# Kernel optimization log

Measured on AMD Instinct MI355X. Metric: run time of the kernel, lower is better.

## Reference

```python
import jax, jax.numpy as jnp
import numpy as np

U, I, D, E, B = 100000, 50000, 128, 3200000, 4096
KEEP_PROB = 0.8

def setup_inputs() -> dict:
    key = jax.random.key(0)
    ks = jax.random.split(key, 9)
    return {
        "user_emb": 0.01 * jax.random.normal(ks[0], (U, D), dtype=jnp.float32),
        "item_emb": 0.01 * jax.random.normal(ks[1], (I, D), dtype=jnp.float32),
        "vals": jax.random.uniform(ks[2], (E,), dtype=jnp.float32),
        "keep_mask": jax.random.uniform(ks[3], (E,), dtype=jnp.float32),
        "rows": jax.random.randint(ks[4], (E,), 0, U, dtype=jnp.int32),
        "cols": jax.random.randint(ks[5], (E,), 0, I, dtype=jnp.int32),
        "user": jax.random.randint(ks[6], (B,), 0, U, dtype=jnp.int32),
        "pos_item": jax.random.randint(ks[7], (B,), 0, I, dtype=jnp.int32),
        "neg_item": jax.random.randint(ks[8], (B,), 0, I, dtype=jnp.int32),
    }

def reference(user_emb, item_emb, vals, keep_mask, rows, cols, user, pos_item, neg_item):
    # Edge dropout: keep edge iff uniform < keep_prob, rescale by 1/keep_prob.
    # (Equivalent to torch's index filtering, expressed as zeroed values.)
    dvals = jnp.where(keep_mask < KEEP_PROB, vals / KEEP_PROB, 0.0)
    u0, i0 = user_emb, item_emb
    # i_1 = spmm(A^T, u_0): scatter edge messages by item (col) index.  [I, D]
    i1 = jax.ops.segment_sum(dvals[:, None] * u0[rows], cols, num_segments=item_emb.shape[0])
    # u_1 = spmm(A, i_0): scatter edge messages by user (row) index.    [U, D]
    u1 = jax.ops.segment_sum(dvals[:, None] * i0[cols], rows, num_segments=user_emb.shape[0])
    # Layer combination (mean of layer-0 and layer-1), gathered per batch.
    u = (u0[user] + u1[user]) * 0.5        # [B, D]
    i = (i0[pos_item] + i1[pos_item]) * 0.5
    j = (i0[neg_item] + i1[neg_item]) * 0.5
    pos_score = jnp.sum(u * i, axis=1, keepdims=True)  # [B, 1]
    neg_score = jnp.sum(u * j, axis=1, keepdims=True)  # [B, 1]
    return (pos_score, neg_score)
```

## Files before the change

kernel.cpp:

```cpp
#include <hip/hip_runtime.h>

#define DIM 128
#define KEEP_PROB 0.8f
#define UCAP 96
#define ICAP 160

__global__ void init_ws_kernel(int4* slots, int slot_vecs, int4* ctrs, int ctr_vecs) {
    int stride = gridDim.x * blockDim.x;
    int t = blockIdx.x * blockDim.x + threadIdx.x;
    int4 m1 = make_int4(-1, -1, -1, -1);
    for (int i = t; i < slot_vecs; i += stride) slots[i] = m1;
    int4 z = make_int4(0, 0, 0, 0);
    for (int i = t; i < ctr_vecs; i += stride) ctrs[i] = z;
}

__global__ void slot_kernel(const int* __restrict__ user, const int* __restrict__ pos,
                            const int* __restrict__ neg, int* __restrict__ u_slot,
                            int* __restrict__ i_slot, int B) {
    int t = blockIdx.x * blockDim.x + threadIdx.x;
    if (t < B) {
        u_slot[user[t]] = t;
    } else if (t < 2 * B) {
        i_slot[pos[t - B]] = t - B;
    } else if (t < 3 * B) {
        i_slot[neg[t - 2 * B]] = (t - 2 * B) + B;
    }
}

__global__ void fill_bucket_kernel(const float* __restrict__ vals, const float* __restrict__ keep,
                                   const int* __restrict__ rows, const int* __restrict__ cols,
                                   const int* __restrict__ u_slot, const int* __restrict__ i_slot,
                                   int* __restrict__ cursor, int2* __restrict__ entries,
                                   int E, int B) {
    int t = blockIdx.x * blockDim.x + threadIdx.x;
    int base = t * 4;
    if (base >= E) return;
    long long ibase = (long long)B * UCAP;
    if (base + 3 < E) {
        float4 km = *(const float4*)(keep + base);
        float4 vv = *(const float4*)(vals + base);
        int4 r4 = *(const int4*)(rows + base);
        int4 c4 = *(const int4*)(cols + base);
        float k[4] = {km.x, km.y, km.z, km.w};
        float v[4] = {vv.x, vv.y, vv.z, vv.w};
        int rr[4] = {r4.x, r4.y, r4.z, r4.w};
        int cc[4] = {c4.x, c4.y, c4.z, c4.w};
#pragma unroll
        for (int j = 0; j < 4; j++) {
            if (k[j] < KEEP_PROB) {
                float dv = v[j] * 1.25f;
                int us = u_slot[rr[j]];
                if (us >= 0) {
                    int p = atomicAdd(&cursor[us], 1);
                    if (p < UCAP) entries[(long long)us * UCAP + p] = make_int2(cc[j], __float_as_int(dv));
                }
                int is = i_slot[cc[j]];
                if (is >= 0) {
                    int p = atomicAdd(&cursor[B + is], 1);
                    if (p < ICAP) entries[ibase + (long long)is * ICAP + p] = make_int2(rr[j], __float_as_int(dv));
                }
            }
        }
    } else {
        for (int e = base; e < E; e++) {
            if (keep[e] < KEEP_PROB) {
                float dv = vals[e] * 1.25f;
                int us = u_slot[rows[e]];
                if (us >= 0) {
                    int p = atomicAdd(&cursor[us], 1);
                    if (p < UCAP) entries[(long long)us * UCAP + p] = make_int2(cols[e], __float_as_int(dv));
                }
                int is = i_slot[cols[e]];
                if (is >= 0) {
                    int p = atomicAdd(&cursor[B + is], 1);
                    if (p < ICAP) entries[ibase + (long long)is * ICAP + p] = make_int2(rows[e], __float_as_int(dv));
                }
            }
        }
    }
}

__global__ void count_kernel(const float* __restrict__ keep, const int* __restrict__ rows,
                             const int* __restrict__ cols, const int* __restrict__ u_slot,
                             const int* __restrict__ i_slot, int* __restrict__ cnt,
                             int E, int B) {
    int t = blockIdx.x * blockDim.x + threadIdx.x;
    int base = t * 4;
    if (base >= E) return;
    if (base + 3 < E) {
        float4 km = *(const float4*)(keep + base);
        int4 r4 = *(const int4*)(rows + base);
        int4 c4 = *(const int4*)(cols + base);
        float k[4] = {km.x, km.y, km.z, km.w};
        int rr[4] = {r4.x, r4.y, r4.z, r4.w};
        int cc[4] = {c4.x, c4.y, c4.z, c4.w};
#pragma unroll
        for (int j = 0; j < 4; j++) {
            if (k[j] < KEEP_PROB) {
                int us = u_slot[rr[j]];
                if (us >= 0) atomicAdd(&cnt[us], 1);
                int is = i_slot[cc[j]];
                if (is >= 0) atomicAdd(&cnt[B + is], 1);
            }
        }
    } else {
        for (int e = base; e < E; e++) {
            if (keep[e] < KEEP_PROB) {
                int us = u_slot[rows[e]];
                if (us >= 0) atomicAdd(&cnt[us], 1);
                int is = i_slot[cols[e]];
                if (is >= 0) atomicAdd(&cnt[B + is], 1);
            }
        }
    }
}

__global__ void scan_kernel(const int* __restrict__ cnt, int* __restrict__ offs,
                            int* __restrict__ cursor, int n) {
    __shared__ int wave_tot[16];
    __shared__ int carry_s;
    int tid = threadIdx.x, lane = tid & 63, wv = tid >> 6;
    if (tid == 0) carry_s = 0;
    __syncthreads();
    for (int base = 0; base < n; base += 1024) {
        int v = (base + tid < n) ? cnt[base + tid] : 0;
        int x = v;
#pragma unroll
        for (int off = 1; off < 64; off <<= 1) {
            int y = __shfl_up(x, off);
            if (lane >= off) x += y;
        }
        if (lane == 63) wave_tot[wv] = x;
        __syncthreads();
        if (wv == 0 && lane < 16) {
            int tot = wave_tot[lane];
            int s = tot;
#pragma unroll
            for (int off = 1; off < 16; off <<= 1) {
                int y = __shfl_up(s, off);
                if (lane >= off) s += y;
            }
            wave_tot[lane] = s - tot;
        }
        __syncthreads();
        int excl = (x - v) + wave_tot[wv] + carry_s;
        if (base + tid < n) { offs[base + tid] = excl; cursor[base + tid] = excl; }
        __syncthreads();
        if (tid == 1023) carry_s += wave_tot[15] + x;
        __syncthreads();
    }
}

__global__ void fill_csr_kernel(const float* __restrict__ vals, const float* __restrict__ keep,
                                const int* __restrict__ rows, const int* __restrict__ cols,
                                const int* __restrict__ u_slot, const int* __restrict__ i_slot,
                                int* __restrict__ cursor, int2* __restrict__ entries,
                                long long cap, int E, int B) {
    int t = blockIdx.x * blockDim.x + threadIdx.x;
    int base = t * 4;
    if (base >= E) return;
    if (base + 3 < E) {
        float4 km = *(const float4*)(keep + base);
        float4 vv = *(const float4*)(vals + base);
        int4 r4 = *(const int4*)(rows + base);
        int4 c4 = *(const int4*)(cols + base);
        float k[4] = {km.x, km.y, km.z, km.w};
        float v[4] = {vv.x, vv.y, vv.z, vv.w};
        int rr[4] = {r4.x, r4.y, r4.z, r4.w};
        int cc[4] = {c4.x, c4.y, c4.z, c4.w};
#pragma unroll
        for (int j = 0; j < 4; j++) {
            if (k[j] < KEEP_PROB) {
                float dv = v[j] * 1.25f;
                int us = u_slot[rr[j]];
                if (us >= 0) {
                    int p = atomicAdd(&cursor[us], 1);
                    if (p < cap) entries[p] = make_int2(cc[j], __float_as_int(dv));
                }
                int is = i_slot[cc[j]];
                if (is >= 0) {
                    int p = atomicAdd(&cursor[B + is], 1);
                    if (p < cap) entries[p] = make_int2(rr[j], __float_as_int(dv));
                }
            }
        }
    } else {
        for (int e = base; e < E; e++) {
            if (keep[e] < KEEP_PROB) {
                float dv = vals[e] * 1.25f;
                int us = u_slot[rows[e]];
                if (us >= 0) {
                    int p = atomicAdd(&cursor[us], 1);
                    if (p < cap) entries[p] = make_int2(cols[e], __float_as_int(dv));
                }
                int is = i_slot[cols[e]];
                if (is >= 0) {
                    int p = atomicAdd(&cursor[B + is], 1);
                    if (p < cap) entries[p] = make_int2(rows[e], __float_as_int(dv));
                }
            }
        }
    }
}

__global__ void gather_kernel(const int2* __restrict__ entries, const int* __restrict__ offs,
                              const int* __restrict__ cntp, const float* __restrict__ u0,
                              const float* __restrict__ i0, float* __restrict__ u1c,
                              float* __restrict__ i1c, int B, int mode, long long cap) {
    int wave = (blockIdx.x * blockDim.x + threadIdx.x) >> 6;
    int lane = threadIdx.x & 63;
    if (wave >= 3 * B) return;
    const float* table;
    float* dst;
    if (wave < B) { table = i0; dst = u1c + (size_t)wave * DIM; }
    else          { table = u0; dst = i1c + (size_t)(wave - B) * DIM; }

    int n = cntp[wave];
    long long base;
    if (mode == 1) {
        if (wave < B) { base = (long long)wave * UCAP; if (n > UCAP) n = UCAP; }
        else          { base = (long long)B * UCAP + (long long)(wave - B) * ICAP; if (n > ICAP) n = ICAP; }
    } else {
        base = offs[wave];
        if (base + n > cap) n = (int)(cap - base < 0 ? 0 : cap - base);
    }

    int o = lane * 2;
    float ax = 0.f, ay = 0.f;
    for (int k0 = 0; k0 < n; k0 += 64) {
        int idx = k0 + lane;
        int2 e = make_int2(0, 0);
        if (idx < n) e = entries[base + idx];
        int m = n - k0;
        if (m > 64) m = 64;
        int j = 0;
        for (; j + 4 <= m; j += 4) {
            int s0 = __shfl(e.x, j + 0), s1 = __shfl(e.x, j + 1);
            int s2 = __shfl(e.x, j + 2), s3 = __shfl(e.x, j + 3);
            float d0 = __int_as_float(__shfl(e.y, j + 0));
            float d1 = __int_as_float(__shfl(e.y, j + 1));
            float d2 = __int_as_float(__shfl(e.y, j + 2));
            float d3 = __int_as_float(__shfl(e.y, j + 3));
            float2 r0 = *(const float2*)(table + (size_t)s0 * DIM + o);
            float2 r1 = *(const float2*)(table + (size_t)s1 * DIM + o);
            float2 r2 = *(const float2*)(table + (size_t)s2 * DIM + o);
            float2 r3 = *(const float2*)(table + (size_t)s3 * DIM + o);
            ax += d0 * r0.x; ay += d0 * r0.y;
            ax += d1 * r1.x; ay += d1 * r1.y;
            ax += d2 * r2.x; ay += d2 * r2.y;
            ax += d3 * r3.x; ay += d3 * r3.y;
        }
        for (; j < m; j++) {
            int s = __shfl(e.x, j);
            float dv = __int_as_float(__shfl(e.y, j));
            float2 r = *(const float2*)(table + (size_t)s * DIM + o);
            ax += dv * r.x; ay += dv * r.y;
        }
    }
    *(float2*)(dst + o) = make_float2(ax, ay);
}

__global__ void score_kernel(const float* __restrict__ u0, const float* __restrict__ i0,
                             const float* __restrict__ u1c, const float* __restrict__ i1c,
                             const int* __restrict__ user, const int* __restrict__ pos,
                             const int* __restrict__ neg, const int* __restrict__ u_slot,
                             const int* __restrict__ i_slot, float* __restrict__ out, int B) {
    int wave = (blockIdx.x * blockDim.x + threadIdx.x) >> 6;
    int lane = threadIdx.x & 63;
    if (wave >= B) return;

    int ub = user[wave], pb = pos[wave], nb = neg[wave];
    int usl = u_slot[ub], psl = i_slot[pb], nsl = i_slot[nb];
    int o = lane * 2;

    float2 a0 = *(const float2*)(u0  + (size_t)ub  * DIM + o);
    float2 a1 = *(const float2*)(u1c + (size_t)usl * DIM + o);
    float2 p0 = *(const float2*)(i0  + (size_t)pb  * DIM + o);
    float2 p1 = *(const float2*)(i1c + (size_t)psl * DIM + o);
    float2 n0 = *(const float2*)(i0  + (size_t)nb  * DIM + o);
    float2 n1 = *(const float2*)(i1c + (size_t)nsl * DIM + o);

    float ux = (a0.x + a1.x) * 0.5f, uy = (a0.y + a1.y) * 0.5f;
    float px = (p0.x + p1.x) * 0.5f, py = (p0.y + p1.y) * 0.5f;
    float nx = (n0.x + n1.x) * 0.5f, ny = (n0.y + n1.y) * 0.5f;

    float ps = ux * px + uy * py;
    float ns = ux * nx + uy * ny;
    for (int off = 32; off > 0; off >>= 1) {
        ps += __shfl_down(ps, off);
        ns += __shfl_down(ns, off);
    }
    if (lane == 0) {
        out[wave]     = ps;
        out[B + wave] = ns;
    }
}

extern "C" void kernel_launch(void* const* d_in, const int* in_sizes, int n_in,
                              void* d_out, int out_size, void* d_ws, size_t ws_size,
                              hipStream_t stream) {
    const float* user_emb = (const float*)d_in[0];
    const float* item_emb = (const float*)d_in[1];
    const float* vals     = (const float*)d_in[2];
    const float* keep     = (const float*)d_in[3];
    const int*   rows     = (const int*)d_in[4];
    const int*   cols     = (const int*)d_in[5];
    const int*   user     = (const int*)d_in[6];
    const int*   pos      = (const int*)d_in[7];
    const int*   neg      = (const int*)d_in[8];
    float* out = (float*)d_out;

    int U = in_sizes[0] / DIM;
    int I = in_sizes[1] / DIM;
    int E = in_sizes[2];
    int B = in_sizes[6];

    char* p = (char*)d_ws;
    int* u_slot = (int*)p;              p += (size_t)U * 4;
    int* i_slot = (int*)p;              p += (size_t)I * 4;
    int* cnt    = (int*)p;              p += (size_t)3 * B * 4;
    int* offs   = (int*)p;              p += (size_t)3 * B * 4;
    int* cursor = (int*)p;              p += (size_t)3 * B * 4;
    float* u1c  = (float*)p;            p += (size_t)B * DIM * 4;
    float* i1c  = (float*)p;            p += (size_t)2 * B * DIM * 4;
    int2* entries = (int2*)p;
    size_t used = (size_t)(p - (char*)d_ws);
    long long avail = (long long)ws_size - (long long)used;

    long long bucket_entries = (long long)B * UCAP + (long long)2 * B * ICAP;
    int mode = (avail >= bucket_entries * (long long)sizeof(int2)) ? 1 : 0;

    int slot_vecs = (U + I) / 4;
    int ctr_vecs  = (9 * B) / 4;

    init_ws_kernel<<<256, 256, 0, stream>>>((int4*)u_slot, slot_vecs, (int4*)cnt, ctr_vecs);
    slot_kernel<<<(3 * B + 255) / 256, 256, 0, stream>>>(user, pos, neg, u_slot, i_slot, B);

    int scan_threads = (E + 3) / 4;
    int scan_blocks = (scan_threads + 255) / 256;

    long long cap;
    if (mode == 1) {
        cap = bucket_entries;
        fill_bucket_kernel<<<scan_blocks, 256, 0, stream>>>(vals, keep, rows, cols, u_slot,
                                                            i_slot, cursor, entries, E, B);
        gather_kernel<<<(3 * B * 64 + 255) / 256, 256, 0, stream>>>(entries, offs, cursor,
                                                                    user_emb, item_emb, u1c,
                                                                    i1c, B, 1, cap);
    } else {
        cap = avail / (long long)sizeof(int2);
        if (cap < 0) cap = 0;
        count_kernel<<<scan_blocks, 256, 0, stream>>>(keep, rows, cols, u_slot, i_slot, cnt, E, B);
        scan_kernel<<<1, 1024, 0, stream>>>(cnt, offs, cursor, 3 * B);
        fill_csr_kernel<<<scan_blocks, 256, 0, stream>>>(vals, keep, rows, cols, u_slot, i_slot,
                                                         cursor, entries, cap, E, B);
        gather_kernel<<<(3 * B * 64 + 255) / 256, 256, 0, stream>>>(entries, offs, cnt,
                                                                    user_emb, item_emb, u1c,
                                                                    i1c, B, 0, cap);
    }

    score_kernel<<<(B * 64 + 255) / 256, 256, 0, stream>>>(user_emb, item_emb, u1c, i1c,
                                                           user, pos, neg, u_slot, i_slot,
                                                           out, B);
}
```

Before: 227.9 us.

## Filter edges with membership bitmasks and split gather rows across two waves

Adds compact bitmasks of the batch users and items, built in the slot kernel. The fill kernel now tests a small, cache-resident bitmask before touching the large slot arrays, and each of its threads handles 8 edges instead of 4. The gather kernel assigns two waves per destination row, interleaving the row's entries between them, unrolling by 8 and combining the two halves through shared memory. The init kernel is replaced by memsets. The fallback CSR kernels are simplified to scalar loops, and the gather grid assumes 3*B is even.

```diff
diff --git a/kernel.cpp b/kernel.cpp
--- a/kernel.cpp
+++ b/kernel.cpp
@@ -5,75 +5,77 @@
 #define UCAP 96
 #define ICAP 160
 
-__global__ void init_ws_kernel(int4* slots, int slot_vecs, int4* ctrs, int ctr_vecs) {
-    int stride = gridDim.x * blockDim.x;
-    int t = blockIdx.x * blockDim.x + threadIdx.x;
-    int4 m1 = make_int4(-1, -1, -1, -1);
-    for (int i = t; i < slot_vecs; i += stride) slots[i] = m1;
-    int4 z = make_int4(0, 0, 0, 0);
-    for (int i = t; i < ctr_vecs; i += stride) ctrs[i] = z;
-}
-
 __global__ void slot_kernel(const int* __restrict__ user, const int* __restrict__ pos,
                             const int* __restrict__ neg, int* __restrict__ u_slot,
-                            int* __restrict__ i_slot, int B) {
+                            int* __restrict__ i_slot, unsigned* __restrict__ u_mask,
+                            unsigned* __restrict__ i_mask, int B) {
     int t = blockIdx.x * blockDim.x + threadIdx.x;
     if (t < B) {
-        u_slot[user[t]] = t;
+        int u = user[t];
+        u_slot[u] = t;
+        atomicOr(&u_mask[u >> 5], 1u << (u & 31));
     } else if (t < 2 * B) {
-        i_slot[pos[t - B]] = t - B;
+        int it = pos[t - B];
+        i_slot[it] = t - B;
+        atomicOr(&i_mask[it >> 5], 1u << (it & 31));
     } else if (t < 3 * B) {
-        i_slot[neg[t - 2 * B]] = (t - 2 * B) + B;
+        int it = neg[t - 2 * B];
+        i_slot[it] = (t - 2 * B) + B;
+        atomicOr(&i_mask[it >> 5], 1u << (it & 31));
     }
 }
 
 __global__ void fill_bucket_kernel(const float* __restrict__ vals, const float* __restrict__ keep,
                                    const int* __restrict__ rows, const int* __restrict__ cols,
                                    const int* __restrict__ u_slot, const int* __restrict__ i_slot,
+                                   const unsigned* __restrict__ u_mask,
+                                   const unsigned* __restrict__ i_mask,
                                    int* __restrict__ cursor, int2* __restrict__ entries,
                                    int E, int B) {
     int t = blockIdx.x * blockDim.x + threadIdx.x;
-    int base = t * 4;
+    int base = t * 8;
     if (base >= E) return;
-    long long ibase = (long long)B * UCAP;
-    if (base + 3 < E) {
-        float4 km = *(const float4*)(keep + base);
-        float4 vv = *(const float4*)(vals + base);
-        int4 r4 = *(const int4*)(rows + base);
-        int4 c4 = *(const int4*)(cols + base);
-        float k[4] = {km.x, km.y, km.z, km.w};
-        float v[4] = {vv.x, vv.y, vv.z, vv.w};
-        int rr[4] = {r4.x, r4.y, r4.z, r4.w};
-        int cc[4] = {c4.x, c4.y, c4.z, c4.w};
+    long long ib = (long long)B * UCAP;
+    if (base + 7 < E) {
+        float4 ka = *(const float4*)(keep + base), kb = *(const float4*)(keep + base + 4);
+        float4 va = *(const float4*)(vals + base), vb = *(const float4*)(vals + base + 4);
+        int4 ra = *(const int4*)(rows + base), rb = *(const int4*)(rows + base + 4);
+        int4 ca = *(const int4*)(cols + base), cb = *(const int4*)(cols + base + 4);
+        float kk[8] = {ka.x, ka.y, ka.z, ka.w, kb.x, kb.y, kb.z, kb.w};
+        float vv[8] = {va.x, va.y, va.z, va.w, vb.x, vb.y, vb.z, vb.w};
+        int rr[8] = {ra.x, ra.y, ra.z, ra.w, rb.x, rb.y, rb.z, rb.w};
+        int cc[8] = {ca.x, ca.y, ca.z, ca.w, cb.x, cb.y, cb.z, cb.w};
 #pragma unroll
-        for (int j = 0; j < 4; j++) {
-            if (k[j] < KEEP_PROB) {
-                float dv = v[j] * 1.25f;
-                int us = u_slot[rr[j]];
-                if (us >= 0) {
+        for (int j = 0; j < 8; j++) {
+            if (kk[j] < KEEP_PROB) {
+                int r = rr[j], c = cc[j];
+                float dv = vv[j] * 1.25f;
+                if ((u_mask[r >> 5] >> (r & 31)) & 1u) {
+                    int us = u_slot[r];
                     int p = atomicAdd(&cursor[us], 1);
-                    if (p < UCAP) entries[(long long)us * UCAP + p] = make_int2(cc[j], __float_as_int(dv));
+                    if (p < UCAP) entries[(long long)us * UCAP + p] = make_int2(c, __float_as_int(dv));
                 }
-                int is = i_slot[cc[j]];
-                if (is >= 0) {
+                if ((i_mask[c >> 5] >> (c & 31)) & 1u) {
+                    int is = i_slot[c];
                     int p = atomicAdd(&cursor[B + is], 1);
-                    if (p < ICAP) entries[ibase + (long long)is * ICAP + p] = make_int2(rr[j], __float_as_int(dv));
+                    if (p < ICAP) entries[ib + (long long)is * ICAP + p] = make_int2(r, __float_as_int(dv));
                 }
             }
         }
     } else {
         for (int e = base; e < E; e++) {
             if (keep[e] < KEEP_PROB) {
+                int r = rows[e], c = cols[e];
                 float dv = vals[e] * 1.25f;
-                int us = u_slot[rows[e]];
-                if (us >= 0) {
+                if ((u_mask[r >> 5] >> (r & 31)) & 1u) {
+                    int us = u_slot[r];
                     int p = atomicAdd(&cursor[us], 1);
-                    if (p < UCAP) entries[(long long)us * UCAP + p] = make_int2(cols[e], __float_as_int(dv));
+                    if (p < UCAP) entries[(long long)us * UCAP + p] = make_int2(c, __float_as_int(dv));
                 }
-                int is = i_slot[cols[e]];
-                if (is >= 0) {
+                if ((i_mask[c >> 5] >> (c & 31)) & 1u) {
+                    int is = i_slot[c];
                     int p = atomicAdd(&cursor[B + is], 1);
-                    if (p < ICAP) entries[ibase + (long long)is * ICAP + p] = make_int2(rows[e], __float_as_int(dv));
+                    if (p < ICAP) entries[ib + (long long)is * ICAP + p] = make_int2(r, __float_as_int(dv));
                 }
             }
         }
@@ -87,30 +89,12 @@
     int t = blockIdx.x * blockDim.x + threadIdx.x;
     int base = t * 4;
     if (base >= E) return;
-    if (base + 3 < E) {
-        float4 km = *(const float4*)(keep + base);
-        int4 r4 = *(const int4*)(rows + base);
-        int4 c4 = *(const int4*)(cols + base);
-        float k[4] = {km.x, km.y, km.z, km.w};
-        int rr[4] = {r4.x, r4.y, r4.z, r4.w};
-        int cc[4] = {c4.x, c4.y, c4.z, c4.w};
-#pragma unroll
-        for (int j = 0; j < 4; j++) {
-            if (k[j] < KEEP_PROB) {
-                int us = u_slot[rr[j]];
-                if (us >= 0) atomicAdd(&cnt[us], 1);
-                int is = i_slot[cc[j]];
-                if (is >= 0) atomicAdd(&cnt[B + is], 1);
-            }
-        }
-    } else {
-        for (int e = base; e < E; e++) {
-            if (keep[e] < KEEP_PROB) {
-                int us = u_slot[rows[e]];
-                if (us >= 0) atomicAdd(&cnt[us], 1);
-                int is = i_slot[cols[e]];
-                if (is >= 0) atomicAdd(&cnt[B + is], 1);
-            }
+    for (int e = base; e < base + 4 && e < E; e++) {
+        if (keep[e] < KEEP_PROB) {
+            int us = u_slot[rows[e]];
+            if (us >= 0) atomicAdd(&cnt[us], 1);
+            int is = i_slot[cols[e]];
+            if (is >= 0) atomicAdd(&cnt[B + is], 1);
         }
     }
 }
@@ -159,45 +143,18 @@
     int t = blockIdx.x * blockDim.x + threadIdx.x;
     int base = t * 4;
     if (base >= E) return;
-    if (base + 3 < E) {
-        float4 km = *(const float4*)(keep + base);
-        float4 vv = *(const float4*)(vals + base);
-        int4 r4 = *(const int4*)(rows + base);
-        int4 c4 = *(const int4*)(cols + base);
-        float k[4] = {km.x, km.y, km.z, km.w};
-        float v[4] = {vv.x, vv.y, vv.z, vv.w};
-        int rr[4] = {r4.x, r4.y, r4.z, r4.w};
-        int cc[4] = {c4.x, c4.y, c4.z, c4.w};
-#pragma unroll
-        for (int j = 0; j < 4; j++) {
-            if (k[j] < KEEP_PROB) {
-                float dv = v[j] * 1.25f;
-                int us = u_slot[rr[j]];
-                if (us >= 0) {
-                    int p = atomicAdd(&cursor[us], 1);
-                    if (p < cap) entries[p] = make_int2(cc[j], __float_as_int(dv));
-                }
-                int is = i_slot[cc[j]];
-                if (is >= 0) {
-                    int p = atomicAdd(&cursor[B + is], 1);
-                    if (p < cap) entries[p] = make_int2(rr[j], __float_as_int(dv));
-                }
-            }
-        }
-    } else {
-        for (int e = base; e < E; e++) {
-            if (keep[e] < KEEP_PROB) {
-                float dv = vals[e] * 1.25f;
-                int us = u_slot[rows[e]];
-                if (us >= 0) {
-                    int p = atomicAdd(&cursor[us], 1);
-                    if (p < cap) entries[p] = make_int2(cols[e], __float_as_int(dv));
-                }
-                int is = i_slot[cols[e]];
-                if (is >= 0) {
-                    int p = atomicAdd(&cursor[B + is], 1);
-                    if (p < cap) entries[p] = make_int2(rows[e], __float_as_int(dv));
-                }
+    for (int e = base; e < base + 4 && e < E; e++) {
+        if (keep[e] < KEEP_PROB) {
+            float dv = vals[e] * 1.25f;
+            int us = u_slot[rows[e]];
+            if (us >= 0) {
+                int p = atomicAdd(&cursor[us], 1);
+                if (p < cap) entries[p] = make_int2(cols[e], __float_as_int(dv));
+            }
+            int is = i_slot[cols[e]];
+            if (is >= 0) {
+                int p = atomicAdd(&cursor[B + is], 1);
+                if (p < cap) entries[p] = make_int2(rows[e], __float_as_int(dv));
             }
         }
     }
@@ -207,57 +164,81 @@
                               const int* __restrict__ cntp, const float* __restrict__ u0,
                               const float* __restrict__ i0, float* __restrict__ u1c,
                               float* __restrict__ i1c, int B, int mode, long long cap) {
-    int wave = (blockIdx.x * blockDim.x + threadIdx.x) >> 6;
+    __shared__ float part[2][DIM];
+    int pair = threadIdx.x >> 7;
+    int half = (threadIdx.x >> 6) & 1;
     int lane = threadIdx.x & 63;
-    if (wave >= 3 * B) return;
+    int dest = blockIdx.x * 2 + pair;
+
     const float* table;
     float* dst;
-    if (wave < B) { table = i0; dst = u1c + (size_t)wave * DIM; }
-    else          { table = u0; dst = i1c + (size_t)(wave - B) * DIM; }
-
-    int n = cntp[wave];
+    if (dest < B) { table = i0; dst = u1c + (size_t)dest * DIM; }
+    else          { table = u0; dst = i1c + (size_t)(dest - B) * DIM; }
+
+    int n = cntp[dest];
     long long base;
     if (mode == 1) {
-        if (wave < B) { base = (long long)wave * UCAP; if (n > UCAP) n = UCAP; }
-        else          { base = (long long)B * UCAP + (long long)(wave - B) * ICAP; if (n > ICAP) n = ICAP; }
+        if (dest < B) { base = (long long)dest * UCAP; if (n > UCAP) n = UCAP; }
+        else { base = (long long)B * UCAP + (long long)(dest - B) * ICAP; if (n > ICAP) n = ICAP; }
     } else {
-        base = offs[wave];
-        if (base + n > cap) n = (int)(cap - base < 0 ? 0 : cap - base);
-    }
-
+        base = offs[dest];
+        if (base + n > cap) { long long rem = cap - base; n = rem < 0 ? 0 : (int)rem; }
+    }
+
+    int m = (n - half + 1) >> 1;
     int o = lane * 2;
     float ax = 0.f, ay = 0.f;
-    for (int k0 = 0; k0 < n; k0 += 64) {
-        int idx = k0 + lane;
+    for (int k0 = 0; k0 < m; k0 += 64) {
+        int my = k0 + lane;
         int2 e = make_int2(0, 0);
-        if (idx < n) e = entries[base + idx];
-        int m = n - k0;
-        if (m > 64) m = 64;
+        if (my < m) e = entries[base + half + 2 * (long long)my];
+        int mm = m - k0;
+        if (mm > 64) mm = 64;
         int j = 0;
-        for (; j + 4 <= m; j += 4) {
+        for (; j + 8 <= mm; j += 8) {
             int s0 = __shfl(e.x, j + 0), s1 = __shfl(e.x, j + 1);
             int s2 = __shfl(e.x, j + 2), s3 = __shfl(e.x, j + 3);
+            int s4 = __shfl(e.x, j + 4), s5 = __shfl(e.x, j + 5);
+            int s6 = __shfl(e.x, j + 6), s7 = __shfl(e.x, j + 7);
             float d0 = __int_as_float(__shfl(e.y, j + 0));
             float d1 = __int_as_float(__shfl(e.y, j + 1));
             float d2 = __int_as_float(__shfl(e.y, j + 2));
             float d3 = __int_as_float(__shfl(e.y, j + 3));
+            float d4 = __int_as_float(__shfl(e.y, j + 4));
+            float d5 = __int_as_float(__shfl(e.y, j + 5));
+            float d6 = __int_as_float(__shfl(e.y, j + 6));
+            float d7 = __int_as_float(__shfl(e.y, j + 7));
             float2 r0 = *(const float2*)(table + (size_t)s0 * DIM + o);
             float2 r1 = *(const float2*)(table + (size_t)s1 * DIM + o);
             float2 r2 = *(const float2*)(table + (size_t)s2 * DIM + o);
             float2 r3 = *(const float2*)(table + (size_t)s3 * DIM + o);
+            float2 r4 = *(const float2*)(table + (size_t)s4 * DIM + o);
+            float2 r5 = *(const float2*)(table + (size_t)s5 * DIM + o);
+            float2 r6 = *(const float2*)(table + (size_t)s6 * DIM + o);
+            float2 r7 = *(const float2*)(table + (size_t)s7 * DIM + o);
             ax += d0 * r0.x; ay += d0 * r0.y;
             ax += d1 * r1.x; ay += d1 * r1.y;
             ax += d2 * r2.x; ay += d2 * r2.y;
             ax += d3 * r3.x; ay += d3 * r3.y;
-        }
-        for (; j < m; j++) {
+            ax += d4 * r4.x; ay += d4 * r4.y;
+            ax += d5 * r5.x; ay += d5 * r5.y;
+            ax += d6 * r6.x; ay += d6 * r6.y;
+            ax += d7 * r7.x; ay += d7 * r7.y;
+        }
+        for (; j < mm; j++) {
             int s = __shfl(e.x, j);
             float dv = __int_as_float(__shfl(e.y, j));
             float2 r = *(const float2*)(table + (size_t)s * DIM + o);
             ax += dv * r.x; ay += dv * r.y;
         }
     }
-    *(float2*)(dst + o) = make_float2(ax, ay);
+    if (half == 1) { part[pair][o] = ax; part[pair][o + 1] = ay; }
+    __syncthreads();
+    if (half == 0) {
+        ax += part[pair][o];
+        ay += part[pair][o + 1];
+        *(float2*)(dst + o) = make_float2(ax, ay);
+    }
 }
 
 __global__ void score_kernel(const float* __restrict__ u0, const float* __restrict__ i0,
@@ -315,9 +296,14 @@
     int E = in_sizes[2];
     int B = in_sizes[6];
 
+    int umw = ((U + 31) / 32 + 3) & ~3;
+    int imw = ((I + 31) / 32 + 3) & ~3;
+
     char* p = (char*)d_ws;
     int* u_slot = (int*)p;              p += (size_t)U * 4;
     int* i_slot = (int*)p;              p += (size_t)I * 4;
+    unsigned* u_mask = (unsigned*)p;    p += (size_t)umw * 4;
+    unsigned* i_mask = (unsigned*)p;    p += (size_t)imw * 4;
     int* cnt    = (int*)p;              p += (size_t)3 * B * 4;
     int* offs   = (int*)p;              p += (size_t)3 * B * 4;
     int* cursor = (int*)p;              p += (size_t)3 * B * 4;
@@ -330,33 +316,30 @@
     long long bucket_entries = (long long)B * UCAP + (long long)2 * B * ICAP;
     int mode = (avail >= bucket_entries * (long long)sizeof(int2)) ? 1 : 0;
 
-    int slot_vecs = (U + I) / 4;
-    int ctr_vecs  = (9 * B) / 4;
-
-    init_ws_kernel<<<256, 256, 0, stream>>>((int4*)u_slot, slot_vecs, (int4*)cnt, ctr_vecs);
-    slot_kernel<<<(3 * B + 255) / 256, 256, 0, stream>>>(user, pos, neg, u_slot, i_slot, B);
-
-    int scan_threads = (E + 3) / 4;
-    int scan_blocks = (scan_threads + 255) / 256;
+    hipMemsetAsync(u_slot, 0xFF, (size_t)(U + I) * 4, stream);
+    hipMemsetAsync(u_mask, 0x00, (size_t)(umw + imw + 9 * B) * 4, stream);
+
+    slot_kernel<<<(3 * B + 255) / 256, 256, 0, stream>>>(user, pos, neg, u_slot, i_slot,
+                                                         u_mask, i_mask, B);
 
     long long cap;
     if (mode == 1) {
         cap = bucket_entries;
-        fill_bucket_kernel<<<scan_blocks, 256, 0, stream>>>(vals, keep, rows, cols, u_slot,
-                                                            i_slot, cursor, entries, E, B);
-        gather_kernel<<<(3 * B * 64 + 255) / 256, 256, 0, stream>>>(entries, offs, cursor,
-                                                                    user_emb, item_emb, u1c,
-                                                                    i1c, B, 1, cap);
+        int fb = ((E + 7) / 8 + 255) / 256;
+        fill_bucket_kernel<<<fb, 256, 0, stream>>>(vals, keep, rows, cols, u_slot, i_slot,
+                                                   u_mask, i_mask, cursor, entries, E, B);
+        gather_kernel<<<(3 * B) / 2, 256, 0, stream>>>(entries, offs, cursor, user_emb,
+                                                       item_emb, u1c, i1c, B, 1, cap);
     } else {
         cap = avail / (long long)sizeof(int2);
         if (cap < 0) cap = 0;
-        count_kernel<<<scan_blocks, 256, 0, stream>>>(keep, rows, cols, u_slot, i_slot, cnt, E, B);
+        int cb = ((E + 3) / 4 + 255) / 256;
+        count_kernel<<<cb, 256, 0, stream>>>(keep, rows, cols, u_slot, i_slot, cnt, E, B);
         scan_kernel<<<1, 1024, 0, stream>>>(cnt, offs, cursor, 3 * B);
-        fill_csr_kernel<<<scan_blocks, 256, 0, stream>>>(vals, keep, rows, cols, u_slot, i_slot,
-                                                         cursor, entries, cap, E, B);
-        gather_kernel<<<(3 * B * 64 + 255) / 256, 256, 0, stream>>>(entries, offs, cnt,
-                                                                    user_emb, item_emb, u1c,
-                                                                    i1c, B, 0, cap);
+        fill_csr_kernel<<<cb, 256, 0, stream>>>(vals, keep, rows, cols, u_slot, i_slot,
+                                                cursor, entries, cap, E, B);
+        gather_kernel<<<(3 * B) / 2, 256, 0, stream>>>(entries, offs, cnt, user_emb,
+                                                       item_emb, u1c, i1c, B, 0, cap);
     }
 
     score_kernel<<<(B * 64 + 255) / 256, 256, 0, stream>>>(user_emb, item_emb, u1c, i1c,
```

Result: faster. 220.2 us (-3.4%).
